# Kernel optimization log

Measured on AMD Instinct MI355X. Metric: run time of the kernel, lower is better.

## Reference

```python
import math
import jax, jax.numpy as jnp
import numpy as np

B, C, H, W = 8, 512, 32, 32
HEADS = 8


def _mix_rot(re, im, Wm, phi):
    # nn.Linear(dim, dim, bias=False) applied channelwise on [B,C,H,W]:
    # y = x @ Wm.T  ->  einsum over input channel c, output channel d
    re2 = jnp.einsum('bchw,dc->bdhw', re, Wm)
    im2 = jnp.einsum('bchw,dc->bdhw', im, Wm)
    c = jnp.cos(phi)[None, :, None, None]
    s = jnp.sin(phi)[None, :, None, None]
    # complex multiply (re2 + i*im2) * (cos phi + i*sin phi)
    return re2 * c - im2 * s, re2 * s + im2 * c


def setup_inputs() -> dict:
    key = jax.random.key(0)
    ks = jax.random.split(key, 6)
    scale = 1.0 / math.sqrt(C)
    return {
        'z_re': jax.random.normal(ks[0], (B, C, H, W), jnp.float32),
        'z_im': jax.random.normal(ks[1], (B, C, H, W), jnp.float32),
        'Wq': jax.random.normal(ks[2], (C, C), jnp.float32) * scale,
        'phi_q': jnp.zeros((C,), jnp.float32),
        'Wk': jax.random.normal(ks[3], (C, C), jnp.float32) * scale,
        'phi_k': jnp.zeros((C,), jnp.float32),
        'Wv': jax.random.normal(ks[4], (C, C), jnp.float32) * scale,
        'phi_v': jnp.zeros((C,), jnp.float32),
        'Wo': jax.random.normal(ks[5], (C, C), jnp.float32) * scale,
        'phi_o': jnp.zeros((C,), jnp.float32),
    }


def reference(z_re, z_im, Wq, phi_q, Wk, phi_k, Wv, phi_v, Wo, phi_o):
    b, c, h, w = z_re.shape
    T = h * w
    dh = c // HEADS

    def tok(a):  # [B,C,H,W] -> [B,T,C]
        return a.reshape(b, c, T).transpose(0, 2, 1)

    qre, qim = _mix_rot(z_re, z_im, Wq, phi_q)
    kre, kim = _mix_rot(z_re, z_im, Wk, phi_k)
    vre, vim = _mix_rot(z_re, z_im, Wv, phi_v)
    qre, qim = tok(qre), tok(qim)
    kre, kim = tok(kre), tok(kim)
    vre, vim = tok(vre), tok(vim)

    # real part of complex inner product: sums over FULL channel dim (no head split)
    scores = (jnp.einsum('btc,buc->btu', qre, kre)
              + jnp.einsum('btc,buc->btu', qim, kim)) / math.sqrt(dh)
    causal = jnp.triu(jnp.ones((T, T), bool), k=1)
    scores = jnp.where(causal[None], -jnp.inf, scores)
    attn = jax.nn.softmax(scores, axis=-1)

    out_re = jnp.einsum('btu,buc->btc', attn, vre)
    out_im = jnp.einsum('btu,buc->btc', attn, vim)

    def grid(a):  # [B,T,C] -> [B,C,H,W]
        return a.transpose(0, 2, 1).reshape(b, c, h, w)

    return _mix_rot(grid(out_re), grid(out_im), Wo, phi_o)
```

## Files before the change

### kernel.cpp

```cpp
#include <hip/hip_runtime.h>
#include <math.h>

#define NB 8
#define NC 512
#define NT 1024
#define BT (NB * NT)
#define SCALE 0.125f
#define NEG_BIG (-3.0e38f)

typedef __attribute__((ext_vector_type(8))) short short8v;
typedef __attribute__((ext_vector_type(8))) _Float16 half8v;
typedef __attribute__((ext_vector_type(4))) float float4v;
#define MFMA_BF16(A, B, C) __builtin_amdgcn_mfma_f32_16x16x32_bf16(A, B, C, 0, 0, 0)
#define MFMA_F16(A, B, C)  __builtin_amdgcn_mfma_f32_16x16x32_f16(A, B, C, 0, 0, 0)

__device__ __forceinline__ ushort f2bf(float f) {
    union { float f; unsigned int i; } v; v.f = f;
    unsigned int r = v.i + 0x7FFFu + ((v.i >> 16) & 1u);
    return (ushort)(r >> 16);
}

__device__ __forceinline__ ushort f2h(float f) {
    return __builtin_bit_cast(unsigned short, (_Float16)f);
}

__device__ __forceinline__ half8v scale8(short8v raw, float s) {
    half8v h = __builtin_bit_cast(half8v, raw);
    const _Float16 hs = (_Float16)s;
    half8v r;
    #pragma unroll
    for (int q = 0; q < 8; ++q) r[q] = h[q] * hs;
    return r;
}

#if defined(__has_builtin)
#if __has_builtin(__builtin_amdgcn_global_load_lds)
#define HAS_GLDS 1
#endif
#endif

#ifdef HAS_GLDS
__device__ __forceinline__ void glds16(const ushort* g, ushort* l) {
    __builtin_amdgcn_global_load_lds(
        (const __attribute__((address_space(1))) unsigned int*)g,
        (__attribute__((address_space(3))) unsigned int*)l, 16, 0, 0);
}
#endif

template<int ROWS>
__device__ __forceinline__ void stage64(const ushort* __restrict__ g, int rsShorts,
                                        ushort* tile, int w, int lane) {
    const int r8 = lane >> 3;
    const int ck = (lane & 7) ^ r8;
    const ushort* gl = g + (size_t)r8 * rsShorts + (ck << 3);
    constexpr int ni = ROWS / 32;
    #pragma unroll
    for (int s = 0; s < ni; ++s) {
        const int issue = w * ni + s;
#ifdef HAS_GLDS
        glds16(gl + (size_t)issue * 8 * rsShorts, tile + issue * 512);
#else
        const uint4 v = *(const uint4*)(gl + (size_t)issue * 8 * rsShorts);
        *(uint4*)(tile + issue * 512 + lane * 8) = v;
#endif
    }
}

__device__ __forceinline__ short8v frag(const ushort* tile, int rr, int q) {
    return *(const short8v*)(tile + rr * 64 + ((q ^ (rr & 7)) << 3));
}

__global__ __launch_bounds__(256) void prep_z_kernel(
    const float* __restrict__ zre, const float* __restrict__ zim,
    ushort* __restrict__ Z)
{
    const int t0 = blockIdx.x << 6, c0 = blockIdx.y << 6;
    const int bz = blockIdx.z, b = bz & 7, comp = bz >> 3;
    const float* src = (comp ? zim : zre) + (size_t)b * NC * NT;
    ushort* dst = Z + (size_t)(comp * NB + b) * NT * NC;
    const int tid = threadIdx.x;

    __shared__ ushort T[64][72];
    #pragma unroll
    for (int r = 0; r < 4; ++r) {
        const int cl = (tid >> 4) + r * 16;
        const int t4 = (tid & 15) << 2;
        const float4 v = *(const float4*)(src + (size_t)(c0 + cl) * NT + t0 + t4);
        T[t4 + 0][cl] = f2bf(v.x); T[t4 + 1][cl] = f2bf(v.y);
        T[t4 + 2][cl] = f2bf(v.z); T[t4 + 3][cl] = f2bf(v.w);
    }
    __syncthreads();
    const int tl = tid >> 2, cc = (tid & 3) << 4;
    ushort* op = dst + (size_t)(t0 + tl) * NC + c0 + cc;
    *(uint4*)op       = *(const uint4*)&T[tl][cc];
    *(uint4*)(op + 8) = *(const uint4*)&T[tl][cc + 8];
}

__global__ __launch_bounds__(256) void prep_w_kernel(
    const float* __restrict__ Wq, const float* __restrict__ Wk,
    const float* __restrict__ Wv, const float* __restrict__ Wo,
    ushort* __restrict__ Wbf)
{
    const int idx = blockIdx.x * 256 + threadIdx.x;
    const int e4 = idx << 2;
    const int m = e4 >> 18;
    const int off = e4 & ((1 << 18) - 1);
    const float* Ws[4] = {Wq, Wk, Wv, Wo};
    const float4 v = *(const float4*)(Ws[m] + off);
    ushort4 o;
    o.x = f2bf(v.x); o.y = f2bf(v.y); o.z = f2bf(v.z); o.w = f2bf(v.w);
    *(ushort4*)(Wbf + ((size_t)m << 18) + off) = o;
}

__global__ __launch_bounds__(256, 2) void proj_qk_kernel(
    const ushort* __restrict__ Z, const ushort* __restrict__ Wbf,
    const float* __restrict__ phiq, const float* __restrict__ phik,
    ushort* __restrict__ qre, ushort* __restrict__ qim,
    ushort* __restrict__ kre, ushort* __restrict__ kim)
{
    const int tid = threadIdx.x;
    const int m0 = blockIdx.x << 7;
    const int d0 = blockIdx.y << 6;
    const size_t NE = (size_t)BT * NC;

    __shared__ alignas(16) ushort Zr[128 * 64], Zi[128 * 64];
    __shared__ alignas(16) ushort Wq_s[64 * 64], Wk_s[64 * 64];

    float4v accq[2][4][2] = {};
    float4v acck[2][4][2] = {};

    const int w = tid >> 6, lane = tid & 63;
    const int l15 = lane & 15, quad = lane >> 4;
    const int wm = (w & 1) << 6;
    const int wn = (w >> 1) << 5;

    for (int c0 = 0; c0 < NC; c0 += 64) {
        stage64<128>(Z + (size_t)m0 * NC + c0, NC, Zr, w, lane);
        stage64<128>(Z + NE + (size_t)m0 * NC + c0, NC, Zi, w, lane);
        stage64<64>(Wbf + (size_t)d0 * NC + c0, NC, Wq_s, w, lane);
        stage64<64>(Wbf + ((size_t)1 << 18) + (size_t)d0 * NC + c0, NC, Wk_s, w, lane);
        __syncthreads();
        #pragma unroll
        for (int kk = 0; kk < 2; ++kk) {
            const int q0 = kk * 4 + quad;
            short8v zf[2][4], wqf[2], wkf[2];
            #pragma unroll
            for (int i = 0; i < 4; ++i) {
                zf[0][i] = frag(Zr, wm + i * 16 + l15, q0);
                zf[1][i] = frag(Zi, wm + i * 16 + l15, q0);
            }
            #pragma unroll
            for (int j = 0; j < 2; ++j) {
                wqf[j] = frag(Wq_s, wn + j * 16 + l15, q0);
                wkf[j] = frag(Wk_s, wn + j * 16 + l15, q0);
            }
            #pragma unroll
            for (int c = 0; c < 2; ++c)
                #pragma unroll
                for (int i = 0; i < 4; ++i)
                    #pragma unroll
                    for (int j = 0; j < 2; ++j) {
                        accq[c][i][j] = MFMA_BF16(zf[c][i], wqf[j], accq[c][i][j]);
                        acck[c][i][j] = MFMA_BF16(zf[c][i], wkf[j], acck[c][i][j]);
                    }
        }
        __syncthreads();
    }

    #pragma unroll
    for (int j = 0; j < 2; ++j) {
        const int d = d0 + wn + j * 16 + l15;
        const float pq = phiq[d], pk = phik[d];
        const float cq = cosf(pq), sq = sinf(pq);
        const float ck = cosf(pk), sk = sinf(pk);
        #pragma unroll
        for (int i = 0; i < 4; ++i)
            #pragma unroll
            for (int r = 0; r < 4; ++r) {
                const size_t m = m0 + wm + i * 16 + quad * 4 + r;
                const size_t off = m * NC + d;
                const float ar = accq[0][i][j][r], ai = accq[1][i][j][r];
                qre[off] = f2bf(ar * cq - ai * sq);
                qim[off] = f2bf(ar * sq + ai * cq);
                const float br = acck[0][i][j][r], bi = acck[1][i][j][r];
                kre[off] = f2bf(br * ck - bi * sk);
                kim[off] = f2bf(br * sk + bi * ck);
            }
    }
}

__global__ __launch_bounds__(256, 3) void proj_v_kernel(
    const ushort* __restrict__ Z, const ushort* __restrict__ Wbf,
    const float* __restrict__ phiv,
    ushort* __restrict__ vre, ushort* __restrict__ vim)
{
    const int tid = threadIdx.x;
    const int d0 = blockIdx.x << 7;
    const int bt0 = blockIdx.y << 6;
    const size_t NE = (size_t)BT * NC;

    __shared__ alignas(16) ushort Wv_s[128 * 64], Zr[64 * 64], Zi[64 * 64];
    float4v acc[2][4][2] = {};

    const int w = tid >> 6, lane = tid & 63;
    const int l15 = lane & 15, quad = lane >> 4;
    const int wm = (w & 1) << 6;
    const int wn = (w >> 1) << 5;

    for (int c0 = 0; c0 < NC; c0 += 64) {
        stage64<128>(Wbf + ((size_t)2 << 18) + (size_t)d0 * NC + c0, NC, Wv_s, w, lane);
        stage64<64>(Z + (size_t)bt0 * NC + c0, NC, Zr, w, lane);
        stage64<64>(Z + NE + (size_t)bt0 * NC + c0, NC, Zi, w, lane);
        __syncthreads();
        #pragma unroll
        for (int kk = 0; kk < 2; ++kk) {
            const int q0 = kk * 4 + quad;
            short8v wvf[4], zf[2][2];
            #pragma unroll
            for (int i = 0; i < 4; ++i)
                wvf[i] = frag(Wv_s, wm + i * 16 + l15, q0);
            #pragma unroll
            for (int j = 0; j < 2; ++j) {
                zf[0][j] = frag(Zr, wn + j * 16 + l15, q0);
                zf[1][j] = frag(Zi, wn + j * 16 + l15, q0);
            }
            #pragma unroll
            for (int c = 0; c < 2; ++c)
                #pragma unroll
                for (int i = 0; i < 4; ++i)
                    #pragma unroll
                    for (int j = 0; j < 2; ++j)
                        acc[c][i][j] = MFMA_BF16(wvf[i], zf[c][j], acc[c][i][j]);
        }
        __syncthreads();
    }

    #pragma unroll
    for (int i = 0; i < 4; ++i)
        #pragma unroll
        for (int r = 0; r < 4; ++r) {
            const int d = d0 + wm + i * 16 + quad * 4 + r;
            const float ph = phiv[d];
            const float cs = cosf(ph), sn = sinf(ph);
            #pragma unroll
            for (int j = 0; j < 2; ++j) {
                const int bt = bt0 + wn + j * 16 + l15;
                const int b = bt >> 10, t = bt & 1023;
                const size_t off = (size_t)b * NC * NT + (size_t)d * NT + t;
                const float vr = acc[0][i][j][r], vi = acc[1][i][j][r];
                vre[off] = f2h(vr * cs - vi * sn);
                vim[off] = f2h(vr * sn + vi * cs);
            }
        }
}

__global__ __launch_bounds__(256, 3) void scores_kernel(
    const ushort* __restrict__ qre, const ushort* __restrict__ qim,
    const ushort* __restrict__ kre, const ushort* __restrict__ kim,
    ushort* __restrict__ Pp, float2* __restrict__ stats)
{
    const int u0b = blockIdx.x << 7;
    const int t0b = (gridDim.y - 1 - blockIdx.y) << 7;
    if (u0b > t0b) return;
    const int b = blockIdx.z;
    const int tid = threadIdx.x;
    const size_t qb = (size_t)b * NT * NC;

    __shared__ alignas(16) ushort Qr[128 * 64], Qi[128 * 64], Kr[128 * 64], Ki[128 * 64];
    float4v acc[4][4] = {};

    const int w = tid >> 6, lane = tid & 63;
    const int l15 = lane & 15, quad = lane >> 4;
    const int wm = (w & 1) << 6;
    const int wn = (w >> 1) << 6;

    for (int c0 = 0; c0 < NC; c0 += 64) {
        stage64<128>(qre + qb + (size_t)t0b * NC + c0, NC, Qr, w, lane);
        stage64<128>(qim + qb + (size_t)t0b * NC + c0, NC, Qi, w, lane);
        stage64<128>(kre + qb + (size_t)u0b * NC + c0, NC, Kr, w, lane);
        stage64<128>(kim + qb + (size_t)u0b * NC + c0, NC, Ki, w, lane);
        __syncthreads();
        #pragma unroll
        for (int kk = 0; kk < 2; ++kk) {
            const int q0 = kk * 4 + quad;
            short8v qf[2][4], kf[2][4];
            #pragma unroll
            for (int i = 0; i < 4; ++i) {
                qf[0][i] = frag(Qr, wm + i * 16 + l15, q0);
                qf[1][i] = frag(Qi, wm + i * 16 + l15, q0);
                kf[0][i] = frag(Kr, wn + i * 16 + l15, q0);
                kf[1][i] = frag(Ki, wn + i * 16 + l15, q0);
            }
            #pragma unroll
            for (int i = 0; i < 4; ++i)
                #pragma unroll
                for (int j = 0; j < 4; ++j) {
                    acc[i][j] = MFMA_BF16(qf[0][i], kf[0][j], acc[i][j]);
                    acc[i][j] = MFMA_BF16(qf[1][i], kf[1][j], acc[i][j]);
                }
        }
        __syncthreads();
    }

    const int sub = (u0b + wn) >> 6;
    float2* st = stats + (size_t)(b * 16 + sub) * NT;
    ushort* Pb = Pp + (size_t)b * NT * NT;
    #pragma unroll
    for (int i = 0; i < 4; ++i)
        #pragma unroll
        for (int r = 0; r < 4; ++r) {
            const int t = t0b + wm + i * 16 + quad * 4 + r;
            float v[4]; float m = NEG_BIG;
            #pragma unroll
            for (int j = 0; j < 4; ++j) {
                const int u = u0b + wn + j * 16 + l15;
                const float x = (u > t) ? NEG_BIG : acc[i][j][r] * SCALE;
                v[j] = x; m = fmaxf(m, x);
            }
            #pragma unroll
            for (int d = 1; d < 16; d <<= 1) m = fmaxf(m, __shfl_xor(m, d, 64));
            float l = 0.f; ushort ph[4];
            #pragma unroll
            for (int j = 0; j < 4; ++j) {
                const float e = __expf(v[j] - m);
                l += e;
                ph[j] = f2h(e);
            }
            #pragma unroll
            for (int d = 1; d < 16; d <<= 1) l += __shfl_xor(l, d, 64);
            ushort* pr = Pb + (size_t)t * NT + u0b + wn + l15;
            #pragma unroll
            for (int j = 0; j < 4; ++j) pr[j * 16] = ph[j];
            if (l15 == 0) st[t] = make_float2(m, l);
        }
}

__global__ __launch_bounds__(256, 3) void pv_kernel(
    const ushort* __restrict__ Pp, const float2* __restrict__ stats,
    const ushort* __restrict__ vre, const ushort* __restrict__ vim,
    ushort* __restrict__ Ore, ushort* __restrict__ Oim)
{
    const int c0b = blockIdx.x << 6;
    const int t0b = (gridDim.y - 1 - blockIdx.y) << 7;
    const int b = blockIdx.z;
    const int tid = threadIdx.x;
    const ushort* P = Pp + ((size_t)b * NT + t0b) * NT;
    const size_t vb = (size_t)b * NC * NT;
    const int iters = (t0b + 128) >> 6;

    __shared__ alignas(16) ushort Ps[128 * 64], Vr[64 * 64], Vi[64 * 64];
    __shared__ float sLds[128][17];
    float4v acc[2][4][2] = {};

    const int w = tid >> 6, lane = tid & 63;
    const int l15 = lane & 15, quad = lane >> 4;
    const int wm = (w & 1) << 6;
    const int wn = (w >> 1) << 5;

    if (tid < 128) {
        const int t = t0b + tid;
        float M = NEG_BIG;
        for (int s = 0; s < iters; ++s)
            M = fmaxf(M, stats[(size_t)(b * 16 + s) * NT + t].x);
        float L = 0.f;
        for (int s = 0; s < iters; ++s) {
            const float2 v = stats[(size_t)(b * 16 + s) * NT + t];
            const float e = __expf(v.x - M);
            sLds[tid][s] = e;
            L += e * v.y;
        }
        const float inv = 1.0f / L;
        for (int s = 0; s < iters; ++s) sLds[tid][s] *= inv;
    }

    for (int it = 0; it < iters; ++it) {
        const int u0 = it << 6;
        stage64<128>(P + u0, NT, Ps, w, lane);
        stage64<64>(vre + vb + (size_t)c0b * NT + u0, NT, Vr, w, lane);
        stage64<64>(vim + vb + (size_t)c0b * NT + u0, NT, Vi, w, lane);
        __syncthreads();
        #pragma unroll
        for (int kk = 0; kk < 2; ++kk) {
            const int q0 = kk * 4 + quad;
            half8v pf[4], vf[2][2];
            #pragma unroll
            for (int i = 0; i < 4; ++i) {
                const int row = wm + i * 16 + l15;
                pf[i] = scale8(frag(Ps, row, q0), sLds[row][it]);
            }
            #pragma unroll
            for (int j = 0; j < 2; ++j) {
                vf[0][j] = __builtin_bit_cast(half8v, frag(Vr, wn + j * 16 + l15, q0));
                vf[1][j] = __builtin_bit_cast(half8v, frag(Vi, wn + j * 16 + l15, q0));
            }
            #pragma unroll
            for (int c = 0; c < 2; ++c)
                #pragma unroll
                for (int i = 0; i < 4; ++i)
                    #pragma unroll
                    for (int j = 0; j < 2; ++j)
                        acc[c][i][j] = MFMA_F16(pf[i], vf[c][j], acc[c][i][j]);
        }
        __syncthreads();
    }
    #pragma unroll
    for (int i = 0; i < 4; ++i)
        #pragma unroll
        for (int j = 0; j < 2; ++j)
            #pragma unroll
            for (int r = 0; r < 4; ++r) {
                const int t = t0b + wm + i * 16 + quad * 4 + r;
                const int c = c0b + wn + j * 16 + l15;
                const size_t off = ((size_t)b * NT + t) * NC + c;
                Ore[off] = f2bf(acc[0][i][j][r]);
                Oim[off] = f2bf(acc[1][i][j][r]);
            }
}

__global__ __launch_bounds__(256, 3) void proj_out_kernel(
    const ushort* __restrict__ Ore, const ushort* __restrict__ Oim,
    const ushort* __restrict__ Wbf, const float* __restrict__ phio,
    float* __restrict__ outRe, float* __restrict__ outIm)
{
    const int tid = threadIdx.x;
    const int d0 = blockIdx.x << 7;
    const int bt0 = blockIdx.y << 6;

    __shared__ alignas(16) ushort Wo_s[128 * 64], Or_s[64 * 64], Oi_s[64 * 64];
    float4v acc[2][4][2] = {};

    const int w = tid >> 6, lane = tid & 63;
    const int l15 = lane & 15, quad = lane >> 4;
    const int wm = (w & 1) << 6;
    const int wn = (w >> 1) << 5;

    for (int c0 = 0; c0 < NC; c0 += 64) {
        stage64<128>(Wbf + ((size_t)3 << 18) + (size_t)d0 * NC + c0, NC, Wo_s, w, lane);
        stage64<64>(Ore + (size_t)bt0 * NC + c0, NC, Or_s, w, lane);
        stage64<64>(Oim + (size_t)bt0 * NC + c0, NC, Oi_s, w, lane);
        __syncthreads();
        #pragma unroll
        for (int kk = 0; kk < 2; ++kk) {
            const int q0 = kk * 4 + quad;
            short8v wof[4], of[2][2];
            #pragma unroll
            for (int i = 0; i < 4; ++i)
                wof[i] = frag(Wo_s, wm + i * 16 + l15, q0);
            #pragma unroll
            for (int j = 0; j < 2; ++j) {
                of[0][j] = frag(Or_s, wn + j * 16 + l15, q0);
                of[1][j] = frag(Oi_s, wn + j * 16 + l15, q0);
            }
            #pragma unroll
            for (int c = 0; c < 2; ++c)
                #pragma unroll
                for (int i = 0; i < 4; ++i)
                    #pragma unroll
                    for (int j = 0; j < 2; ++j)
                        acc[c][i][j] = MFMA_BF16(wof[i], of[c][j], acc[c][i][j]);
        }
        __syncthreads();
    }

    #pragma unroll
    for (int i = 0; i < 4; ++i)
        #pragma unroll
        for (int r = 0; r < 4; ++r) {
            const int d = d0 + wm + i * 16 + quad * 4 + r;
            const float ph = phio[d];
            const float cs = cosf(ph), sn = sinf(ph);
            #pragma unroll
            for (int j = 0; j < 2; ++j) {
                const int bt = bt0 + wn + j * 16 + l15;
                const int b = bt >> 10, t = bt & 1023;
                const size_t off = (size_t)b * NC * NT + (size_t)d * NT + t;
                const float re2 = acc[0][i][j][r], im2 = acc[1][i][j][r];
                outRe[off] = re2 * cs - im2 * sn;
                outIm[off] = re2 * sn + im2 * cs;
            }
        }
}

extern "C" void kernel_launch(void* const* d_in, const int* in_sizes, int n_in,
                              void* d_out, int out_size, void* d_ws, size_t ws_size,
                              hipStream_t stream) {
    (void)in_sizes; (void)n_in; (void)out_size; (void)ws_size;
    const float* z_re  = (const float*)d_in[0];
    const float* z_im  = (const float*)d_in[1];
    const float* Wq    = (const float*)d_in[2];
    const float* phi_q = (const float*)d_in[3];
    const float* Wk    = (const float*)d_in[4];
    const float* phi_k = (const float*)d_in[5];
    const float* Wv    = (const float*)d_in[6];
    const float* phi_v = (const float*)d_in[7];
    const float* Wo    = (const float*)d_in[8];
    const float* phi_o = (const float*)d_in[9];

    const size_t NE = (size_t)BT * NC;
    ushort* ws  = (ushort*)d_ws;
    ushort* qre = ws + 0 * NE; ushort* qim = ws + 1 * NE;
    ushort* kre = ws + 2 * NE; ushort* kim = ws + 3 * NE;
    ushort* vre = ws + 4 * NE; ushort* vim = ws + 5 * NE;
    ushort* Wbf = ws + 6 * NE;
    ushort* Z  = (ushort*)d_out;
    ushort* Pp = (ushort*)d_out + 2 * NE;
    float2* stats = (float2*)d_out;

    const dim3 blk(256);
    hipLaunchKernelGGL(prep_z_kernel, dim3(NT / 64, NC / 64, NB * 2), blk, 0, stream, z_re, z_im, Z);
    hipLaunchKernelGGL(prep_w_kernel, dim3(1024), blk, 0, stream, Wq, Wk, Wv, Wo, Wbf);
    hipLaunchKernelGGL(proj_qk_kernel, dim3(BT / 128, NC / 64), blk, 0, stream,
                       Z, Wbf, phi_q, phi_k, qre, qim, kre, kim);
    hipLaunchKernelGGL(proj_v_kernel, dim3(NC / 128, BT / 64), blk, 0, stream,
                       Z, Wbf, phi_v, vre, vim);
    hipLaunchKernelGGL(scores_kernel, dim3(NT / 128, NT / 128, NB), blk, 0, stream,
                       qre, qim, kre, kim, Pp, stats);
    hipLaunchKernelGGL(pv_kernel, dim3(NC / 64, NT / 128, NB), blk, 0, stream,
                       Pp, stats, vre, vim, qre, qim);
    hipLaunchKernelGGL(proj_out_kernel, dim3(NC / 128, BT / 64), blk, 0, stream,
                       qre, qim, Wbf, phi_o, (float*)d_out, (float*)d_out + NE);
}
```

Measured before the change: 233.9 us.

## Switch all GEMM kernels from 16x16x32 to 32x32x16 MFMA tiles

```diff
diff --git a/kernel.cpp b/kernel.cpp
--- a/kernel.cpp
+++ b/kernel.cpp
@@ -10,9 +10,9 @@
 
 typedef __attribute__((ext_vector_type(8))) short short8v;
 typedef __attribute__((ext_vector_type(8))) _Float16 half8v;
-typedef __attribute__((ext_vector_type(4))) float float4v;
-#define MFMA_BF16(A, B, C) __builtin_amdgcn_mfma_f32_16x16x32_bf16(A, B, C, 0, 0, 0)
-#define MFMA_F16(A, B, C)  __builtin_amdgcn_mfma_f32_16x16x32_f16(A, B, C, 0, 0, 0)
+typedef __attribute__((ext_vector_type(16))) float float16v;
+#define MFMA32_BF16(A, B, C) __builtin_amdgcn_mfma_f32_32x32x16_bf16(A, B, C, 0, 0, 0)
+#define MFMA32_F16(A, B, C)  __builtin_amdgcn_mfma_f32_32x32x16_f16(A, B, C, 0, 0, 0)
 
 __device__ __forceinline__ ushort f2bf(float f) {
     union { float f; unsigned int i; } v; v.f = f;
@@ -68,6 +68,10 @@
 
 __device__ __forceinline__ short8v frag(const ushort* tile, int rr, int q) {
     return *(const short8v*)(tile + rr * 64 + ((q ^ (rr & 7)) << 3));
+}
+
+__device__ __forceinline__ int crow(int r, int h) {
+    return (r & 3) + 8 * (r >> 2) + 4 * h;
 }
 
 __global__ __launch_bounds__(256) void prep_z_kernel(
@@ -126,11 +130,11 @@
     __shared__ alignas(16) ushort Zr[128 * 64], Zi[128 * 64];
     __shared__ alignas(16) ushort Wq_s[64 * 64], Wk_s[64 * 64];
 
-    float4v accq[2][4][2] = {};
-    float4v acck[2][4][2] = {};
+    float16v accq[2][2] = {};
+    float16v acck[2][2] = {};
 
     const int w = tid >> 6, lane = tid & 63;
-    const int l15 = lane & 15, quad = lane >> 4;
+    const int l31 = lane & 31, h = lane >> 5;
     const int wm = (w & 1) << 6;
     const int wn = (w >> 1) << 5;
 
@@ -141,52 +145,44 @@
         stage64<64>(Wbf + ((size_t)1 << 18) + (size_t)d0 * NC + c0, NC, Wk_s, w, lane);
         __syncthreads();
         #pragma unroll
-        for (int kk = 0; kk < 2; ++kk) {
-            const int q0 = kk * 4 + quad;
-            short8v zf[2][4], wqf[2], wkf[2];
-            #pragma unroll
-            for (int i = 0; i < 4; ++i) {
-                zf[0][i] = frag(Zr, wm + i * 16 + l15, q0);
-                zf[1][i] = frag(Zi, wm + i * 16 + l15, q0);
-            }
-            #pragma unroll
-            for (int j = 0; j < 2; ++j) {
-                wqf[j] = frag(Wq_s, wn + j * 16 + l15, q0);
-                wkf[j] = frag(Wk_s, wn + j * 16 + l15, q0);
-            }
+        for (int ks = 0; ks < 4; ++ks) {
+            const int q0 = ks * 2 + h;
+            short8v zf[2][2], wqf, wkf;
+            #pragma unroll
+            for (int i = 0; i < 2; ++i) {
+                zf[0][i] = frag(Zr, wm + i * 32 + l31, q0);
+                zf[1][i] = frag(Zi, wm + i * 32 + l31, q0);
+            }
+            wqf = frag(Wq_s, wn + l31, q0);
+            wkf = frag(Wk_s, wn + l31, q0);
             #pragma unroll
             for (int c = 0; c < 2; ++c)
                 #pragma unroll
-                for (int i = 0; i < 4; ++i)
-                    #pragma unroll
-                    for (int j = 0; j < 2; ++j) {
-                        accq[c][i][j] = MFMA_BF16(zf[c][i], wqf[j], accq[c][i][j]);
-                        acck[c][i][j] = MFMA_BF16(zf[c][i], wkf[j], acck[c][i][j]);
-                    }
-        }
-        __syncthreads();
-    }
-
-    #pragma unroll
-    for (int j = 0; j < 2; ++j) {
-        const int d = d0 + wn + j * 16 + l15;
-        const float pq = phiq[d], pk = phik[d];
-        const float cq = cosf(pq), sq = sinf(pq);
-        const float ck = cosf(pk), sk = sinf(pk);
-        #pragma unroll
-        for (int i = 0; i < 4; ++i)
-            #pragma unroll
-            for (int r = 0; r < 4; ++r) {
-                const size_t m = m0 + wm + i * 16 + quad * 4 + r;
-                const size_t off = m * NC + d;
-                const float ar = accq[0][i][j][r], ai = accq[1][i][j][r];
-                qre[off] = f2bf(ar * cq - ai * sq);
-                qim[off] = f2bf(ar * sq + ai * cq);
-                const float br = acck[0][i][j][r], bi = acck[1][i][j][r];
-                kre[off] = f2bf(br * ck - bi * sk);
-                kim[off] = f2bf(br * sk + bi * ck);
-            }
-    }
+                for (int i = 0; i < 2; ++i) {
+                    accq[c][i] = MFMA32_BF16(zf[c][i], wqf, accq[c][i]);
+                    acck[c][i] = MFMA32_BF16(zf[c][i], wkf, acck[c][i]);
+                }
+        }
+        __syncthreads();
+    }
+
+    const int d = d0 + wn + l31;
+    const float pq = phiq[d], pk = phik[d];
+    const float cq = cosf(pq), sq = sinf(pq);
+    const float ck = cosf(pk), sk = sinf(pk);
+    #pragma unroll
+    for (int i = 0; i < 2; ++i)
+        #pragma unroll
+        for (int r = 0; r < 16; ++r) {
+            const size_t m = m0 + wm + i * 32 + crow(r, h);
+            const size_t off = m * NC + d;
+            const float ar = accq[0][i][r], ai = accq[1][i][r];
+            qre[off] = f2bf(ar * cq - ai * sq);
+            qim[off] = f2bf(ar * sq + ai * cq);
+            const float br = acck[0][i][r], bi = acck[1][i][r];
+            kre[off] = f2bf(br * ck - bi * sk);
+            kim[off] = f2bf(br * sk + bi * ck);
+        }
 }
 
 __global__ __launch_bounds__(256, 3) void proj_v_kernel(
@@ -200,10 +196,10 @@
     const size_t NE = (size_t)BT * NC;
 
     __shared__ alignas(16) ushort Wv_s[128 * 64], Zr[64 * 64], Zi[64 * 64];
-    float4v acc[2][4][2] = {};
+    float16v acc[2][2] = {};
 
     const int w = tid >> 6, lane = tid & 63;
-    const int l15 = lane & 15, quad = lane >> 4;
+    const int l31 = lane & 31, h = lane >> 5;
     const int wm = (w & 1) << 6;
     const int wn = (w >> 1) << 5;
 
@@ -213,44 +209,36 @@
         stage64<64>(Z + NE + (size_t)bt0 * NC + c0, NC, Zi, w, lane);
         __syncthreads();
         #pragma unroll
-        for (int kk = 0; kk < 2; ++kk) {
-            const int q0 = kk * 4 + quad;
-            short8v wvf[4], zf[2][2];
-            #pragma unroll
-            for (int i = 0; i < 4; ++i)
-                wvf[i] = frag(Wv_s, wm + i * 16 + l15, q0);
-            #pragma unroll
-            for (int j = 0; j < 2; ++j) {
-                zf[0][j] = frag(Zr, wn + j * 16 + l15, q0);
-                zf[1][j] = frag(Zi, wn + j * 16 + l15, q0);
-            }
-            #pragma unroll
-            for (int c = 0; c < 2; ++c)
-                #pragma unroll
-                for (int i = 0; i < 4; ++i)
-                    #pragma unroll
-                    for (int j = 0; j < 2; ++j)
-                        acc[c][i][j] = MFMA_BF16(wvf[i], zf[c][j], acc[c][i][j]);
-        }
-        __syncthreads();
-    }
-
-    #pragma unroll
-    for (int i = 0; i < 4; ++i)
-        #pragma unroll
-        for (int r = 0; r < 4; ++r) {
-            const int d = d0 + wm + i * 16 + quad * 4 + r;
+        for (int ks = 0; ks < 4; ++ks) {
+            const int q0 = ks * 2 + h;
+            short8v wvf[2], zfr, zfi;
+            #pragma unroll
+            for (int i = 0; i < 2; ++i)
+                wvf[i] = frag(Wv_s, wm + i * 32 + l31, q0);
+            zfr = frag(Zr, wn + l31, q0);
+            zfi = frag(Zi, wn + l31, q0);
+            #pragma unroll
+            for (int i = 0; i < 2; ++i) {
+                acc[0][i] = MFMA32_BF16(wvf[i], zfr, acc[0][i]);
+                acc[1][i] = MFMA32_BF16(wvf[i], zfi, acc[1][i]);
+            }
+        }
+        __syncthreads();
+    }
+
+    const int bt = bt0 + wn + l31;
+    const int b = bt >> 10, t = bt & 1023;
+    #pragma unroll
+    for (int i = 0; i < 2; ++i)
+        #pragma unroll
+        for (int r = 0; r < 16; ++r) {
+            const int d = d0 + wm + i * 32 + crow(r, h);
             const float ph = phiv[d];
             const float cs = cosf(ph), sn = sinf(ph);
-            #pragma unroll
-            for (int j = 0; j < 2; ++j) {
-                const int bt = bt0 + wn + j * 16 + l15;
-                const int b = bt >> 10, t = bt & 1023;
-                const size_t off = (size_t)b * NC * NT + (size_t)d * NT + t;
-                const float vr = acc[0][i][j][r], vi = acc[1][i][j][r];
-                vre[off] = f2h(vr * cs - vi * sn);
-                vim[off] = f2h(vr * sn + vi * cs);
-            }
+            const size_t off = (size_t)b * NC * NT + (size_t)d * NT + t;
+            const float vr = acc[0][i][r], vi = acc[1][i][r];
+            vre[off] = f2h(vr * cs - vi * sn);
+            vim[off] = f2h(vr * sn + vi * cs);
         }
 }
 
@@ -267,10 +255,10 @@
     const size_t qb = (size_t)b * NT * NC;
 
     __shared__ alignas(16) ushort Qr[128 * 64], Qi[128 * 64], Kr[128 * 64], Ki[128 * 64];
-    float4v acc[4][4] = {};
+    float16v acc[2][2] = {};
 
     const int w = tid >> 6, lane = tid & 63;
-    const int l15 = lane & 15, quad = lane >> 4;
+    const int l31 = lane & 31, h = lane >> 5;
     const int wm = (w & 1) << 6;
     const int wn = (w >> 1) << 6;
 
@@ -281,22 +269,22 @@
         stage64<128>(kim + qb + (size_t)u0b * NC + c0, NC, Ki, w, lane);
         __syncthreads();
         #pragma unroll
-        for (int kk = 0; kk < 2; ++kk) {
-            const int q0 = kk * 4 + quad;
-            short8v qf[2][4], kf[2][4];
-            #pragma unroll
-            for (int i = 0; i < 4; ++i) {
-                qf[0][i] = frag(Qr, wm + i * 16 + l15, q0);
-                qf[1][i] = frag(Qi, wm + i * 16 + l15, q0);
-                kf[0][i] = frag(Kr, wn + i * 16 + l15, q0);
-                kf[1][i] = frag(Ki, wn + i * 16 + l15, q0);
-            }
-            #pragma unroll
-            for (int i = 0; i < 4; ++i)
+        for (int ks = 0; ks < 4; ++ks) {
+            const int q0 = ks * 2 + h;
+            short8v qf[2][2], kf[2][2];
+            #pragma unroll
+            for (int i = 0; i < 2; ++i) {
+                qf[0][i] = frag(Qr, wm + i * 32 + l31, q0);
+                qf[1][i] = frag(Qi, wm + i * 32 + l31, q0);
+                kf[0][i] = frag(Kr, wn + i * 32 + l31, q0);
+                kf[1][i] = frag(Ki, wn + i * 32 + l31, q0);
+            }
+            #pragma unroll
+            for (int i = 0; i < 2; ++i)
                 #pragma unroll
-                for (int j = 0; j < 4; ++j) {
-                    acc[i][j] = MFMA_BF16(qf[0][i], kf[0][j], acc[i][j]);
-                    acc[i][j] = MFMA_BF16(qf[1][i], kf[1][j], acc[i][j]);
+                for (int j = 0; j < 2; ++j) {
+                    acc[i][j] = MFMA32_BF16(qf[0][i], kf[0][j], acc[i][j]);
+                    acc[i][j] = MFMA32_BF16(qf[1][i], kf[1][j], acc[i][j]);
                 }
         }
         __syncthreads();
@@ -306,32 +294,32 @@
     float2* st = stats + (size_t)(b * 16 + sub) * NT;
     ushort* Pb = Pp + (size_t)b * NT * NT;
     #pragma unroll
-    for (int i = 0; i < 4; ++i)
-        #pragma unroll
-        for (int r = 0; r < 4; ++r) {
-            const int t = t0b + wm + i * 16 + quad * 4 + r;
-            float v[4]; float m = NEG_BIG;
-            #pragma unroll
-            for (int j = 0; j < 4; ++j) {
-                const int u = u0b + wn + j * 16 + l15;
+    for (int i = 0; i < 2; ++i)
+        #pragma unroll
+        for (int r = 0; r < 16; ++r) {
+            const int t = t0b + wm + i * 32 + crow(r, h);
+            float v[2]; float m = NEG_BIG;
+            #pragma unroll
+            for (int j = 0; j < 2; ++j) {
+                const int u = u0b + wn + j * 32 + l31;
                 const float x = (u > t) ? NEG_BIG : acc[i][j][r] * SCALE;
                 v[j] = x; m = fmaxf(m, x);
             }
             #pragma unroll
-            for (int d = 1; d < 16; d <<= 1) m = fmaxf(m, __shfl_xor(m, d, 64));
-            float l = 0.f; ushort ph[4];
-            #pragma unroll
-            for (int j = 0; j < 4; ++j) {
+            for (int d = 1; d < 32; d <<= 1) m = fmaxf(m, __shfl_xor(m, d, 64));
+            float l = 0.f; ushort ph[2];
+            #pragma unroll
+            for (int j = 0; j < 2; ++j) {
                 const float e = __expf(v[j] - m);
                 l += e;
                 ph[j] = f2h(e);
             }
             #pragma unroll
-            for (int d = 1; d < 16; d <<= 1) l += __shfl_xor(l, d, 64);
-            ushort* pr = Pb + (size_t)t * NT + u0b + wn + l15;
-            #pragma unroll
-            for (int j = 0; j < 4; ++j) pr[j * 16] = ph[j];
-            if (l15 == 0) st[t] = make_float2(m, l);
+            for (int d = 1; d < 32; d <<= 1) l += __shfl_xor(l, d, 64);
+            ushort* pr = Pb + (size_t)t * NT + u0b + wn + l31;
+            pr[0]  = ph[0];
+            pr[32] = ph[1];
+            if (l31 == 0) st[t] = make_float2(m, l);
         }
 }
 
@@ -350,27 +338,32 @@
 
     __shared__ alignas(16) ushort Ps[128 * 64], Vr[64 * 64], Vi[64 * 64];
     __shared__ float sLds[128][17];
-    float4v acc[2][4][2] = {};
+    float16v acc[2][2] = {};
 
     const int w = tid >> 6, lane = tid & 63;
-    const int l15 = lane & 15, quad = lane >> 4;
+    const int l31 = lane & 31, h = lane >> 5;
     const int wm = (w & 1) << 6;
     const int wn = (w >> 1) << 5;
 
     if (tid < 128) {
         const int t = t0b + tid;
+        float mv[16], lv[16];
+        #pragma unroll
+        for (int s = 0; s < 16; ++s) {
+            if (s < iters) {
+                const float2 v = stats[(size_t)(b * 16 + s) * NT + t];
+                mv[s] = v.x; lv[s] = v.y;
+            } else { mv[s] = NEG_BIG; lv[s] = 0.f; }
+        }
         float M = NEG_BIG;
-        for (int s = 0; s < iters; ++s)
-            M = fmaxf(M, stats[(size_t)(b * 16 + s) * NT + t].x);
-        float L = 0.f;
-        for (int s = 0; s < iters; ++s) {
-            const float2 v = stats[(size_t)(b * 16 + s) * NT + t];
-            const float e = __expf(v.x - M);
-            sLds[tid][s] = e;
-            L += e * v.y;
-        }
+        #pragma unroll
+        for (int s = 0; s < 16; ++s) M = fmaxf(M, mv[s]);
+        float L = 0.f; float ev[16];
+        #pragma unroll
+        for (int s = 0; s < 16; ++s) { ev[s] = __expf(mv[s] - M); L += ev[s] * lv[s]; }
         const float inv = 1.0f / L;
-        for (int s = 0; s < iters; ++s) sLds[tid][s] *= inv;
+        #pragma unroll
+        for (int s = 0; s < 16; ++s) sLds[tid][s] = ev[s] * inv;
     }
 
     for (int it = 0; it < iters; ++it) {
@@ -380,41 +373,35 @@
         stage64<64>(vim + vb + (size_t)c0b * NT + u0, NT, Vi, w, lane);
         __syncthreads();
         #pragma unroll
-        for (int kk = 0; kk < 2; ++kk) {
-            const int q0 = kk * 4 + quad;
-            half8v pf[4], vf[2][2];
-            #pragma unroll
-            for (int i = 0; i < 4; ++i) {
-                const int row = wm + i * 16 + l15;
+        for (int ks = 0; ks < 4; ++ks) {
+            const int q0 = ks * 2 + h;
+            half8v pf[2], vfr, vfi;
+            #pragma unroll
+            for (int i = 0; i < 2; ++i) {
+                const int row = wm + i * 32 + l31;
                 pf[i] = scale8(frag(Ps, row, q0), sLds[row][it]);
             }
-            #pragma unroll
-            for (int j = 0; j < 2; ++j) {
-                vf[0][j] = __builtin_bit_cast(half8v, frag(Vr, wn + j * 16 + l15, q0));
-                vf[1][j] = __builtin_bit_cast(half8v, frag(Vi, wn + j * 16 + l15, q0));
-            }
-            #pragma unroll
-            for (int c = 0; c < 2; ++c)
-                #pragma unroll
-                for (int i = 0; i < 4; ++i)
-                    #pragma unroll
-                    for (int j = 0; j < 2; ++j)
-                        acc[c][i][j] = MFMA_F16(pf[i], vf[c][j], acc[c][i][j]);
-        }
-        __syncthreads();
-    }
-    #pragma unroll
-    for (int i = 0; i < 4; ++i)
-        #pragma unroll
-        for (int j = 0; j < 2; ++j)
-            #pragma unroll
-            for (int r = 0; r < 4; ++r) {
-                const int t = t0b + wm + i * 16 + quad * 4 + r;
-                const int c = c0b + wn + j * 16 + l15;
-                const size_t off = ((size_t)b * NT + t) * NC + c;
-                Ore[off] = f2bf(acc[0][i][j][r]);
-                Oim[off] = f2bf(acc[1][i][j][r]);
-            }
+            vfr = __builtin_bit_cast(half8v, frag(Vr, wn + l31, q0));
+            vfi = __builtin_bit_cast(half8v, frag(Vi, wn + l31, q0));
+            #pragma unroll
+            for (int i = 0; i < 2; ++i) {
+                acc[0][i] = MFMA32_F16(pf[i], vfr, acc[0][i]);
+                acc[1][i] = MFMA32_F16(pf[i], vfi, acc[1][i]);
+            }
+        }
+        __syncthreads();
+    }
+
+    const int c = c0b + wn + l31;
+    #pragma unroll
+    for (int i = 0; i < 2; ++i)
+        #pragma unroll
+        for (int r = 0; r < 16; ++r) {
+            const int t = t0b + wm + i * 32 + crow(r, h);
+            const size_t off = ((size_t)b * NT + t) * NC + c;
+            Ore[off] = f2bf(acc[0][i][r]);
+            Oim[off] = f2bf(acc[1][i][r]);
+        }
 }
 
 __global__ __launch_bounds__(256, 3) void proj_out_kernel(
@@ -427,10 +414,10 @@
     const int bt0 = blockIdx.y << 6;
 
     __shared__ alignas(16) ushort Wo_s[128 * 64], Or_s[64 * 64], Oi_s[64 * 64];
-    float4v acc[2][4][2] = {};
+    float16v acc[2][2] = {};
 
     const int w = tid >> 6, lane = tid & 63;
-    const int l15 = lane & 15, quad = lane >> 4;
+    const int l31 = lane & 31, h = lane >> 5;
     const int wm = (w & 1) << 6;
     const int wn = (w >> 1) << 5;
 
@@ -440,44 +427,36 @@
         stage64<64>(Oim + (size_t)bt0 * NC + c0, NC, Oi_s, w, lane);
         __syncthreads();
         #pragma unroll
-        for (int kk = 0; kk < 2; ++kk) {
-            const int q0 = kk * 4 + quad;
-            short8v wof[4], of[2][2];
-            #pragma unroll
-            for (int i = 0; i < 4; ++i)
-                wof[i] = frag(Wo_s, wm + i * 16 + l15, q0);
-            #pragma unroll
-            for (int j = 0; j < 2; ++j) {
-                of[0][j] = frag(Or_s, wn + j * 16 + l15, q0);
-                of[1][j] = frag(Oi_s, wn + j * 16 + l15, q0);
-            }
-            #pragma unroll
-            for (int c = 0; c < 2; ++c)
-                #pragma unroll
-                for (int i = 0; i < 4; ++i)
-                    #pragma unroll
-                    for (int j = 0; j < 2; ++j)
-                        acc[c][i][j] = MFMA_BF16(wof[i], of[c][j], acc[c][i][j]);
-        }
-        __syncthreads();
-    }
-
-    #pragma unroll
-    for (int i = 0; i < 4; ++i)
-        #pragma unroll
-        for (int r = 0; r < 4; ++r) {
-            const int d = d0 + wm + i * 16 + quad * 4 + r;
+        for (int ks = 0; ks < 4; ++ks) {
+            const int q0 = ks * 2 + h;
+            short8v wof[2], ofr, ofi;
+            #pragma unroll
+            for (int i = 0; i < 2; ++i)
+                wof[i] = frag(Wo_s, wm + i * 32 + l31, q0);
+            ofr = frag(Or_s, wn + l31, q0);
+            ofi = frag(Oi_s, wn + l31, q0);
+            #pragma unroll
+            for (int i = 0; i < 2; ++i) {
+                acc[0][i] = MFMA32_BF16(wof[i], ofr, acc[0][i]);
+                acc[1][i] = MFMA32_BF16(wof[i], ofi, acc[1][i]);
+            }
+        }
+        __syncthreads();
+    }
+
+    const int bt = bt0 + wn + l31;
+    const int b = bt >> 10, t = bt & 1023;
+    #pragma unroll
+    for (int i = 0; i < 2; ++i)
+        #pragma unroll
+        for (int r = 0; r < 16; ++r) {
+            const int d = d0 + wm + i * 32 + crow(r, h);
             const float ph = phio[d];
             const float cs = cosf(ph), sn = sinf(ph);
-            #pragma unroll
-            for (int j = 0; j < 2; ++j) {
-                const int bt = bt0 + wn + j * 16 + l15;
-                const int b = bt >> 10, t = bt & 1023;
-                const size_t off = (size_t)b * NC * NT + (size_t)d * NT + t;
-                const float re2 = acc[0][i][j][r], im2 = acc[1][i][j][r];
-                outRe[off] = re2 * cs - im2 * sn;
-                outIm[off] = re2 * sn + im2 * cs;
-            }
+            const size_t off = (size_t)b * NC * NT + (size_t)d * NT + t;
+            const float re2 = acc[0][i][r], im2 = acc[1][i][r];
+            outRe[off] = re2 * cs - im2 * sn;
+            outIm[off] = re2 * sn + im2 * cs;
         }
 }
 
```

Result: slower. 364.4 us (+55.8%).

## Shrink scores tile to 128x64 to skip more causal-masked work; unroll stats merge

Applied to the files above, without the earlier changes.

```diff
diff --git a/kernel.cpp b/kernel.cpp
--- a/kernel.cpp
+++ b/kernel.cpp
@@ -259,40 +259,42 @@
     const ushort* __restrict__ kre, const ushort* __restrict__ kim,
     ushort* __restrict__ Pp, float2* __restrict__ stats)
 {
-    const int u0b = blockIdx.x << 7;
+    const int u0b = blockIdx.x << 6;
     const int t0b = (gridDim.y - 1 - blockIdx.y) << 7;
-    if (u0b > t0b) return;
+    if (u0b > t0b + 64) return;
     const int b = blockIdx.z;
     const int tid = threadIdx.x;
     const size_t qb = (size_t)b * NT * NC;
 
-    __shared__ alignas(16) ushort Qr[128 * 64], Qi[128 * 64], Kr[128 * 64], Ki[128 * 64];
-    float4v acc[4][4] = {};
+    __shared__ alignas(16) ushort Qr[128 * 64], Qi[128 * 64], Kr[64 * 64], Ki[64 * 64];
+    float4v acc[2][4] = {};
 
     const int w = tid >> 6, lane = tid & 63;
     const int l15 = lane & 15, quad = lane >> 4;
-    const int wm = (w & 1) << 6;
-    const int wn = (w >> 1) << 6;
+    const int wm = w << 5;
 
     for (int c0 = 0; c0 < NC; c0 += 64) {
         stage64<128>(qre + qb + (size_t)t0b * NC + c0, NC, Qr, w, lane);
         stage64<128>(qim + qb + (size_t)t0b * NC + c0, NC, Qi, w, lane);
-        stage64<128>(kre + qb + (size_t)u0b * NC + c0, NC, Kr, w, lane);
-        stage64<128>(kim + qb + (size_t)u0b * NC + c0, NC, Ki, w, lane);
+        stage64<64>(kre + qb + (size_t)u0b * NC + c0, NC, Kr, w, lane);
+        stage64<64>(kim + qb + (size_t)u0b * NC + c0, NC, Ki, w, lane);
         __syncthreads();
         #pragma unroll
         for (int kk = 0; kk < 2; ++kk) {
             const int q0 = kk * 4 + quad;
-            short8v qf[2][4], kf[2][4];
-            #pragma unroll
-            for (int i = 0; i < 4; ++i) {
+            short8v qf[2][2], kf[2][4];
+            #pragma unroll
+            for (int i = 0; i < 2; ++i) {
                 qf[0][i] = frag(Qr, wm + i * 16 + l15, q0);
                 qf[1][i] = frag(Qi, wm + i * 16 + l15, q0);
-                kf[0][i] = frag(Kr, wn + i * 16 + l15, q0);
-                kf[1][i] = frag(Ki, wn + i * 16 + l15, q0);
-            }
-            #pragma unroll
-            for (int i = 0; i < 4; ++i)
+            }
+            #pragma unroll
+            for (int j = 0; j < 4; ++j) {
+                kf[0][j] = frag(Kr, j * 16 + l15, q0);
+                kf[1][j] = frag(Ki, j * 16 + l15, q0);
+            }
+            #pragma unroll
+            for (int i = 0; i < 2; ++i)
                 #pragma unroll
                 for (int j = 0; j < 4; ++j) {
                     acc[i][j] = MFMA_BF16(qf[0][i], kf[0][j], acc[i][j]);
@@ -302,18 +304,18 @@
         __syncthreads();
     }
 
-    const int sub = (u0b + wn) >> 6;
+    const int sub = u0b >> 6;
     float2* st = stats + (size_t)(b * 16 + sub) * NT;
     ushort* Pb = Pp + (size_t)b * NT * NT;
     #pragma unroll
-    for (int i = 0; i < 4; ++i)
+    for (int i = 0; i < 2; ++i)
         #pragma unroll
         for (int r = 0; r < 4; ++r) {
             const int t = t0b + wm + i * 16 + quad * 4 + r;
             float v[4]; float m = NEG_BIG;
             #pragma unroll
             for (int j = 0; j < 4; ++j) {
-                const int u = u0b + wn + j * 16 + l15;
+                const int u = u0b + j * 16 + l15;
                 const float x = (u > t) ? NEG_BIG : acc[i][j][r] * SCALE;
                 v[j] = x; m = fmaxf(m, x);
             }
@@ -328,7 +330,7 @@
             }
             #pragma unroll
             for (int d = 1; d < 16; d <<= 1) l += __shfl_xor(l, d, 64);
-            ushort* pr = Pb + (size_t)t * NT + u0b + wn + l15;
+            ushort* pr = Pb + (size_t)t * NT + u0b + l15;
             #pragma unroll
             for (int j = 0; j < 4; ++j) pr[j * 16] = ph[j];
             if (l15 == 0) st[t] = make_float2(m, l);
@@ -359,18 +361,23 @@
 
     if (tid < 128) {
         const int t = t0b + tid;
+        float mv[16], lv[16];
+        #pragma unroll
+        for (int s = 0; s < 16; ++s) {
+            if (s < iters) {
+                const float2 v = stats[(size_t)(b * 16 + s) * NT + t];
+                mv[s] = v.x; lv[s] = v.y;
+            } else { mv[s] = NEG_BIG; lv[s] = 0.f; }
+        }
         float M = NEG_BIG;
-        for (int s = 0; s < iters; ++s)
-            M = fmaxf(M, stats[(size_t)(b * 16 + s) * NT + t].x);
-        float L = 0.f;
-        for (int s = 0; s < iters; ++s) {
-            const float2 v = stats[(size_t)(b * 16 + s) * NT + t];
-            const float e = __expf(v.x - M);
-            sLds[tid][s] = e;
-            L += e * v.y;
-        }
+        #pragma unroll
+        for (int s = 0; s < 16; ++s) M = fmaxf(M, mv[s]);
+        float L = 0.f; float ev[16];
+        #pragma unroll
+        for (int s = 0; s < 16; ++s) { ev[s] = __expf(mv[s] - M); L += ev[s] * lv[s]; }
         const float inv = 1.0f / L;
-        for (int s = 0; s < iters; ++s) sLds[tid][s] *= inv;
+        #pragma unroll
+        for (int s = 0; s < 16; ++s) sLds[tid][s] = ev[s] * inv;
     }
 
     for (int it = 0; it < iters; ++it) {
@@ -513,7 +520,7 @@
                        Z, Wbf, phi_q, phi_k, qre, qim, kre, kim);
     hipLaunchKernelGGL(proj_v_kernel, dim3(NC / 128, BT / 64), blk, 0, stream,
                        Z, Wbf, phi_v, vre, vim);
-    hipLaunchKernelGGL(scores_kernel, dim3(NT / 128, NT / 128, NB), blk, 0, stream,
+    hipLaunchKernelGGL(scores_kernel, dim3(NT / 64, NT / 128, NB), blk, 0, stream,
                        qre, qim, kre, kim, Pp, stats);
     hipLaunchKernelGGL(pv_kernel, dim3(NC / 64, NT / 128, NB), blk, 0, stream,
                        Pp, stats, vre, vim, qre, qim);
```

Measured after the change: 235.8 us. Within noise of the previous version (+0.8%).
